# Kernel tuning notes

Hardware: AMD Instinct MI355X
Metric: run time of the kernel (lower is better)

Reference implementation:

```python
import jax, jax.numpy as jnp
import numpy as np

B, S, D = 4, 2048, 1024
LN_EPS = 1e-5
GATE_EPS = 1e-9


def _layernorm(x, g, b):
    m = jnp.mean(x, axis=-1, keepdims=True)
    v = jnp.var(x, axis=-1, keepdims=True)
    return (x - m) * jax.lax.rsqrt(v + LN_EPS) * g + b


def setup_inputs() -> dict:
    key = jax.random.key(0)
    ks = jax.random.split(key, 6)
    return {
        "x": jax.random.normal(ks[0], (B, S, D), jnp.float32),
        "ln1_g": jnp.ones((D,), jnp.float32),
        "ln1_b": jnp.zeros((D,), jnp.float32),
        # stacked per-projection params, order (q, k, v, o)
        "mu_w": 0.02 * jax.random.normal(ks[1], (4, D, D), jnp.float32),
        "mu_b": jnp.zeros((4, D), jnp.float32),
        "proto_w": 0.02 * jax.random.normal(ks[2], (4, D, D), jnp.float32),
        "gate": 0.02 * jax.random.normal(ks[3], (4, D), jnp.float32),
        "pt_w": 0.02 * jax.random.normal(ks[4], (4, D, D), jnp.float32),
        "pln_g": jnp.ones((4, D), jnp.float32),
        "pln_b": jnp.zeros((4, D), jnp.float32),
        "in_proto": 0.02 * jax.random.normal(ks[5], (4, D, D), jnp.float32),
    }


def reference(x, ln1_g, ln1_b, mu_w, mu_b, proto_w, gate, pt_w, pln_g, pln_b, in_proto):
    d = x.shape[-1]
    scale = 1.0 / jnp.sqrt(jnp.asarray(d, x.dtype))

    # proto-state update: proto_weight + LayerNorm(Linear(incoming_proto_state))
    prc = jnp.einsum("ned,nfd->nef", in_proto, pt_w)  # [4,D,D]
    proto_state = proto_w + _layernorm(prc, pln_g[:, None, :], pln_b[:, None, :])

    h = _layernorm(x, ln1_g, ln1_b)  # [B,S,D]

    # SparseProtoLinear for q,k,v (stacked): SiLU GEMM + proto match GEMM
    comp = jax.nn.silu(jnp.einsum("bsd,nfd->nbsf", h, mu_w[:3]) + mu_b[:3, None, None, :])
    mv = jnp.einsum("bsd,nfd->nbsf", h, proto_state[:3]) * scale
    g3 = gate[:3]
    cost = g3 / (jnp.max(jnp.abs(g3), axis=-1, keepdims=True) + GATE_EPS)  # [3,D]
    logits = mv - cost[:, None, None, :]
    masked = comp * (logits > 0)  # hard gate (no grad through mask)
    q, k, v = masked[0], masked[1], masked[2]

    # single-head causal attention, head_dim = d_model
    scores = jnp.einsum("bqd,bkd->bqk", q, k) * scale  # [B,S,S]
    causal = jnp.tril(jnp.ones((scores.shape[-2], scores.shape[-1]), bool))
    scores = jnp.where(causal, scores, jnp.asarray(-jnp.inf, scores.dtype))
    attn = jax.nn.softmax(scores, axis=-1)
    attn_out = jnp.einsum("bqk,bkd->bqd", attn, v)  # [B,S,D]

    # output SparseProtoLinear + gating
    c_o = jax.nn.silu(attn_out @ mu_w[3].T + mu_b[3])
    mv_o = (attn_out @ proto_state[3].T) * scale
    cost_o = gate[3] / (jnp.max(jnp.abs(gate[3])) + GATE_EPS)
    masked_o = c_o * ((mv_o - cost_o) > 0)

    return x + masked_o
```

## Files before the change

### kernel.cpp

```cpp
#include <hip/hip_runtime.h>
#include <math.h>

#define Dd 1024
#define Ss 2048
#define NBATCH 4
#define LDSP 4096

static constexpr size_t SDsz = (size_t)Ss * Dd;
static constexpr size_t MIsz = (size_t)Dd * Dd;
static constexpr size_t SSsz = (size_t)Ss * Ss;
static constexpr float LN_EPS_ = 1e-5f;
static constexpr float GATE_EPS_ = 1e-9f;
static constexpr float SCALE_ = 1.0f / 32.0f;

typedef _Float16 f16;
typedef _Float16 f16x8 __attribute__((ext_vector_type(8)));
typedef _Float16 f16x4 __attribute__((ext_vector_type(4)));
typedef float f32x4 __attribute__((ext_vector_type(4)));

__device__ __forceinline__ float silu_f(float v) { return v / (1.0f + __expf(-v)); }

__device__ __forceinline__ void split2(float x, f16& a, f16& b) {
  a = (f16)x; b = (f16)(x - (float)a);
}

__device__ __forceinline__ int swz(int r, int c) {
  return r * 32 + ((c ^ ((r >> 1) & 3)) << 3);
}

__device__ __forceinline__ float2 block_sum2(float2 v) {
#pragma unroll
  for (int o = 32; o > 0; o >>= 1) { v.x += __shfl_down(v.x, o); v.y += __shfl_down(v.y, o); }
  __shared__ float2 sm2[4];
  if ((threadIdx.x & 63) == 0) sm2[threadIdx.x >> 6] = v;
  __syncthreads();
  float2 r; r.x = sm2[0].x + sm2[1].x + sm2[2].x + sm2[3].x;
  r.y = sm2[0].y + sm2[1].y + sm2[2].y + sm2[3].y;
  __syncthreads();
  return r;
}
__device__ __forceinline__ float block_sum1(float v) {
#pragma unroll
  for (int o = 32; o > 0; o >>= 1) v += __shfl_down(v, o);
  __shared__ float sm1[4];
  if ((threadIdx.x & 63) == 0) sm1[threadIdx.x >> 6] = v;
  __syncthreads();
  float r = sm1[0] + sm1[1] + sm1[2] + sm1[3];
  __syncthreads();
  return r;
}
__device__ __forceinline__ float block_max1(float v) {
#pragma unroll
  for (int o = 32; o > 0; o >>= 1) v = fmaxf(v, __shfl_down(v, o));
  __shared__ float smm[4];
  if ((threadIdx.x & 63) == 0) smm[threadIdx.x >> 6] = v;
  __syncthreads();
  float r = fmaxf(fmaxf(smm[0], smm[1]), fmaxf(smm[2], smm[3]));
  __syncthreads();
  return r;
}

template<int PLANES, int MAXSUM>
__device__ __forceinline__ void mp_core(
    f16* __restrict__ smem,
    const f16* __restrict__ Ap0, const f16* __restrict__ Ap1,
    const f16* __restrict__ Bp0, const f16* __restrict__ Bp1,
    int lda, int ldb, int m0, int n0, int kt_end, f32x4 acc[4][4]) {
  const f16* Ap[2] = {Ap0, Ap1};
  const f16* Bp[2] = {Bp0, Bp1};
  const int tid = threadIdx.x;
  const int l = tid & 63;
  const int wv = tid >> 6;
  const int wr = (wv >> 1) * 64, wc = (wv & 1) * 64;
  const int fl = l & 15, fq = l >> 4;
  const int r0 = tid >> 2, cc = tid & 3, kc = cc * 8;

  f16x8 ra[PLANES][2], rb[PLANES][2];
#pragma unroll
  for (int p = 0; p < PLANES; ++p) {
    ra[p][0] = *(const f16x8*)(Ap[p] + (size_t)(m0 + r0) * lda + kc);
    ra[p][1] = *(const f16x8*)(Ap[p] + (size_t)(m0 + 64 + r0) * lda + kc);
    rb[p][0] = *(const f16x8*)(Bp[p] + (size_t)(n0 + r0) * ldb + kc);
    rb[p][1] = *(const f16x8*)(Bp[p] + (size_t)(n0 + 64 + r0) * ldb + kc);
  }
  for (int kt = 0; kt < kt_end; ++kt) {
    __syncthreads();
#pragma unroll
    for (int p = 0; p < PLANES; ++p) {
      *(f16x8*)(smem + p * LDSP + swz(r0, cc)) = ra[p][0];
      *(f16x8*)(smem + p * LDSP + swz(64 + r0, cc)) = ra[p][1];
      *(f16x8*)(smem + (PLANES + p) * LDSP + swz(r0, cc)) = rb[p][0];
      *(f16x8*)(smem + (PLANES + p) * LDSP + swz(64 + r0, cc)) = rb[p][1];
    }
    __syncthreads();
    if (kt + 1 < kt_end) {
      const int ko = (kt + 1) * 32 + kc;
#pragma unroll
      for (int p = 0; p < PLANES; ++p) {
        ra[p][0] = *(const f16x8*)(Ap[p] + (size_t)(m0 + r0) * lda + ko);
        ra[p][1] = *(const f16x8*)(Ap[p] + (size_t)(m0 + 64 + r0) * lda + ko);
        rb[p][0] = *(const f16x8*)(Bp[p] + (size_t)(n0 + r0) * ldb + ko);
        rb[p][1] = *(const f16x8*)(Bp[p] + (size_t)(n0 + 64 + r0) * ldb + ko);
      }
    }
    f16x8 af[PLANES][4];
#pragma unroll
    for (int p = 0; p < PLANES; ++p)
#pragma unroll
      for (int fr = 0; fr < 4; ++fr)
        af[p][fr] = *(const f16x8*)(smem + p * LDSP + swz(wr + fr * 16 + fl, fq));
#pragma unroll
    for (int fc = 0; fc < 4; ++fc) {
      f16x8 bf[PLANES];
#pragma unroll
      for (int p = 0; p < PLANES; ++p)
        bf[p] = *(const f16x8*)(smem + (PLANES + p) * LDSP + swz(wc + fc * 16 + fl, fq));
#pragma unroll
      for (int i = 0; i < PLANES; ++i)
#pragma unroll
        for (int j = 0; j < PLANES; ++j)
          if (i + j <= MAXSUM) {
#pragma unroll
            for (int fr = 0; fr < 4; ++fr)
              acc[fr][fc] = __builtin_amdgcn_mfma_f32_16x16x32_f16(af[i][fr], bf[j], acc[fr][fc], 0, 0, 0);
          }
    }
  }
}

__device__ __forceinline__ void fused_core(
    f16* __restrict__ smem,
    const f16* __restrict__ A0p, const f16* __restrict__ A1p,
    const f16* __restrict__ W0p, const f16* __restrict__ W1p,
    const f16* __restrict__ P0p, const f16* __restrict__ P1p,
    int lda, int ldb, int m0, int n0, int kt_end,
    f32x4 acc1[4][4], f32x4 acc2[4][4]) {
  const f16* As[2] = {A0p, A1p};
  const f16* Bs[4] = {W0p, W1p, P0p, P1p};
  const int tid = threadIdx.x;
  const int l = tid & 63;
  const int wv = tid >> 6;
  const int wr = (wv >> 1) * 64, wc = (wv & 1) * 64;
  const int fl = l & 15, fq = l >> 4;
  const int r0 = tid >> 2, cc = tid & 3, kc = cc * 8;

  f16x8 ra[2][2], rb[4][2];
#pragma unroll
  for (int p = 0; p < 2; ++p) {
    ra[p][0] = *(const f16x8*)(As[p] + (size_t)(m0 + r0) * lda + kc);
    ra[p][1] = *(const f16x8*)(As[p] + (size_t)(m0 + 64 + r0) * lda + kc);
  }
#pragma unroll
  for (int p = 0; p < 4; ++p) {
    rb[p][0] = *(const f16x8*)(Bs[p] + (size_t)(n0 + r0) * ldb + kc);
    rb[p][1] = *(const f16x8*)(Bs[p] + (size_t)(n0 + 64 + r0) * ldb + kc);
  }
  for (int kt = 0; kt < kt_end; ++kt) {
    __syncthreads();
#pragma unroll
    for (int p = 0; p < 2; ++p) {
      *(f16x8*)(smem + p * LDSP + swz(r0, cc)) = ra[p][0];
      *(f16x8*)(smem + p * LDSP + swz(64 + r0, cc)) = ra[p][1];
    }
#pragma unroll
    for (int p = 0; p < 4; ++p) {
      *(f16x8*)(smem + (2 + p) * LDSP + swz(r0, cc)) = rb[p][0];
      *(f16x8*)(smem + (2 + p) * LDSP + swz(64 + r0, cc)) = rb[p][1];
    }
    __syncthreads();
    if (kt + 1 < kt_end) {
      const int ko = (kt + 1) * 32 + kc;
#pragma unroll
      for (int p = 0; p < 2; ++p) {
        ra[p][0] = *(const f16x8*)(As[p] + (size_t)(m0 + r0) * lda + ko);
        ra[p][1] = *(const f16x8*)(As[p] + (size_t)(m0 + 64 + r0) * lda + ko);
      }
#pragma unroll
      for (int p = 0; p < 4; ++p) {
        rb[p][0] = *(const f16x8*)(Bs[p] + (size_t)(n0 + r0) * ldb + ko);
        rb[p][1] = *(const f16x8*)(Bs[p] + (size_t)(n0 + 64 + r0) * ldb + ko);
      }
    }
    f16x8 af0[4], af1[4];
#pragma unroll
    for (int fr = 0; fr < 4; ++fr) {
      af0[fr] = *(const f16x8*)(smem + 0 * LDSP + swz(wr + fr * 16 + fl, fq));
      af1[fr] = *(const f16x8*)(smem + 1 * LDSP + swz(wr + fr * 16 + fl, fq));
    }
#pragma unroll
    for (int fc = 0; fc < 4; ++fc) {
      f16x8 bw0 = *(const f16x8*)(smem + 2 * LDSP + swz(wc + fc * 16 + fl, fq));
      f16x8 bw1 = *(const f16x8*)(smem + 3 * LDSP + swz(wc + fc * 16 + fl, fq));
      f16x8 bp0 = *(const f16x8*)(smem + 4 * LDSP + swz(wc + fc * 16 + fl, fq));
      f16x8 bp1 = *(const f16x8*)(smem + 5 * LDSP + swz(wc + fc * 16 + fl, fq));
#pragma unroll
      for (int fr = 0; fr < 4; ++fr) {
        acc1[fr][fc] = __builtin_amdgcn_mfma_f32_16x16x32_f16(af0[fr], bw0, acc1[fr][fc], 0, 0, 0);
        acc2[fr][fc] = __builtin_amdgcn_mfma_f32_16x16x32_f16(af0[fr], bp0, acc2[fr][fc], 0, 0, 0);
        acc1[fr][fc] = __builtin_amdgcn_mfma_f32_16x16x32_f16(af0[fr], bw1, acc1[fr][fc], 0, 0, 0);
        acc2[fr][fc] = __builtin_amdgcn_mfma_f32_16x16x32_f16(af0[fr], bp1, acc2[fr][fc], 0, 0, 0);
        acc1[fr][fc] = __builtin_amdgcn_mfma_f32_16x16x32_f16(af1[fr], bw0, acc1[fr][fc], 0, 0, 0);
        acc2[fr][fc] = __builtin_amdgcn_mfma_f32_16x16x32_f16(af1[fr], bp0, acc2[fr][fc], 0, 0, 0);
      }
    }
  }
}

template<class F>
__device__ __forceinline__ void epilogue(const f32x4 acc[4][4], int m0, int n0, F&& f) {
  const int tid = threadIdx.x;
  const int l = tid & 63;
  const int wv = tid >> 6;
  const int wr = (wv >> 1) * 64, wc = (wv & 1) * 64;
  const int fl = l & 15, fq = l >> 4;
#pragma unroll
  for (int fr = 0; fr < 4; ++fr)
#pragma unroll
    for (int fc = 0; fc < 4; ++fc) {
      f32x4 av = acc[fr][fc];
#pragma unroll
      for (int r = 0; r < 4; ++r)
        f(m0 + wr + fr * 16 + fq * 4 + r, n0 + wc + fc * 16 + fl, av[r]);
    }
}
template<class F>
__device__ __forceinline__ void epilogue2(const f32x4 a1[4][4], const f32x4 a2[4][4], int m0, int n0, F&& f) {
  const int tid = threadIdx.x;
  const int l = tid & 63;
  const int wv = tid >> 6;
  const int wr = (wv >> 1) * 64, wc = (wv & 1) * 64;
  const int fl = l & 15, fq = l >> 4;
#pragma unroll
  for (int fr = 0; fr < 4; ++fr)
#pragma unroll
    for (int fc = 0; fc < 4; ++fc) {
      f32x4 v1 = a1[fr][fc], v2 = a2[fr][fc];
#pragma unroll
      for (int r = 0; r < 4; ++r)
        f(m0 + wr + fr * 16 + fq * 4 + r, n0 + wc + fc * 16 + fl, v1[r], v2[r]);
    }
}


__global__ __launch_bounds__(256, 3) void k_prc(const f16* __restrict__ ip0, const f16* __restrict__ ip1,
                                                const f16* __restrict__ pt0, const f16* __restrict__ pt1,
                                                float* __restrict__ prc) {
  __shared__ f16 smem[4 * LDSP];
  const int n = blockIdx.z;
  const int m0 = blockIdx.x * 128, n0 = blockIdx.y * 128;
  const size_t o = (size_t)n * MIsz;
  f32x4 acc[4][4] = {};
  mp_core<2, 2>(smem, ip0 + o, ip1 + o, pt0 + o, pt1 + o, Dd, Dd, m0, n0, Dd / 32, acc);
  float* Cp = prc + o;
  epilogue(acc, m0, n0, [&](int row, int col, float aval) {
    Cp[(size_t)row * Dd + col] = aval;
  });
}

__global__ __launch_bounds__(256, 2) void k_fqkv(const f16* __restrict__ h0, const f16* __restrict__ h1,
                                                 const f16* __restrict__ w0, const f16* __restrict__ w1,
                                                 const f16* __restrict__ s0, const f16* __restrict__ s1,
                                                 const float* __restrict__ mu_b, const float* __restrict__ cost,
                                                 f16* __restrict__ qkvb, int C) {
  __shared__ f16 smem[6 * LDSP];
  const int z = blockIdx.z, n = z / C, cb = z - n * C;
  const int m0 = blockIdx.x * 128, n0 = blockIdx.y * 128;
  const size_t ao = (size_t)cb * SDsz, bo = (size_t)n * MIsz;
  f32x4 acc1[4][4] = {}, acc2[4][4] = {};
  fused_core(smem, h0 + ao, h1 + ao, w0 + bo, w1 + bo, s0 + bo, s1 + bo,
             Dd, Dd, m0, n0, Dd / 32, acc1, acc2);
  const float* bp = mu_b + (size_t)n * Dd;
  const float* cp = cost + (size_t)n * Dd;
  f16* o0 = qkvb + ((size_t)(2 * n) * C + cb) * SDsz;
  f16* o1 = qkvb + ((size_t)(2 * n + 1) * C + cb) * SDsz;
  epilogue2(acc1, acc2, m0, n0, [&](int row, int col, float v1, float v2) {
    bool m = (v2 * SCALE_ - cp[col]) > 0.f;
    float comp = m ? silu_f(v1 + bp[col]) : 0.f;
    f16 lo, hi; split2(comp, lo, hi);
    size_t idx = (size_t)row * Dd + col;
    o0[idx] = lo; o1[idx] = hi;
  });
}

__global__ __launch_bounds__(256, 3) void k_scores(const f16* __restrict__ qkvb, float* __restrict__ scores, int C) {
  const int m0 = blockIdx.x * 128, n0 = blockIdx.y * 128;
  if (n0 >= m0 + 128) return;
  __shared__ f16 smem[4 * LDSP];
  const int cb = blockIdx.z;
  const f16* q0 = qkvb + ((size_t)0 * C + cb) * SDsz;
  const f16* q1 = qkvb + ((size_t)1 * C + cb) * SDsz;
  const f16* kk0 = qkvb + ((size_t)2 * C + cb) * SDsz;
  const f16* kk1 = qkvb + ((size_t)3 * C + cb) * SDsz;
  f32x4 acc[4][4] = {};
  mp_core<2, 1>(smem, q0, q1, kk0, kk1, Dd, Dd, m0, n0, Dd / 32, acc);
  float* Cp = scores + (size_t)cb * SSsz;
  epilogue(acc, m0, n0, [&](int row, int col, float aval) {
    Cp[(size_t)row * Ss + col] = aval * SCALE_;
  });
}

__global__ __launch_bounds__(256, 3) void k_pv(const f16* __restrict__ a0, const f16* __restrict__ a1,
                                               const f16* __restrict__ vT0, const f16* __restrict__ vT1,
                                               f16* __restrict__ ao0, f16* __restrict__ ao1) {
  __shared__ f16 smem[4 * LDSP];
  const int cb = blockIdx.z;
  const int m0 = blockIdx.x * 128, n0 = blockIdx.y * 128;
  const f16* A0 = a0 + (size_t)cb * SSsz;
  const f16* A1 = a1 + (size_t)cb * SSsz;
  const f16* B0 = vT0 + (size_t)cb * SDsz;
  const f16* B1 = vT1 + (size_t)cb * SDsz;
  const int kt_end = (m0 + 128) / 32;
  f32x4 acc[4][4] = {};
  mp_core<2, 1>(smem, A0, A1, B0, B1, Ss, Ss, m0, n0, kt_end, acc);
  f16* p0 = ao0 + (size_t)cb * SDsz;
  f16* p1 = ao1 + (size_t)cb * SDsz;
  epilogue(acc, m0, n0, [&](int row, int col, float aval) {
    f16 x0, x1; split2(aval, x0, x1);
    size_t idx = (size_t)row * Dd + col;
    p0[idx] = x0; p1[idx] = x1;
  });
}

__global__ __launch_bounds__(256, 2) void k_fout(const f16* __restrict__ ao0, const f16* __restrict__ ao1,
                                                 const f16* __restrict__ w30, const f16* __restrict__ w31,
                                                 const f16* __restrict__ s30, const f16* __restrict__ s31,
                                                 const float* __restrict__ b3, const float* __restrict__ cost3,
                                                 const float* __restrict__ x, float* __restrict__ out, int b0) {
  __shared__ f16 smem[6 * LDSP];
  const int cb = blockIdx.z;
  const int m0 = blockIdx.x * 128, n0 = blockIdx.y * 128;
  const size_t ao = (size_t)cb * SDsz;
  f32x4 acc1[4][4] = {}, acc2[4][4] = {};
  fused_core(smem, ao0 + ao, ao1 + ao, w30, w31, s30, s31,
             Dd, Dd, m0, n0, Dd / 32, acc1, acc2);
  const float* xp = x + (size_t)(b0 + cb) * SDsz;
  float* op = out + (size_t)(b0 + cb) * SDsz;
  epilogue2(acc1, acc2, m0, n0, [&](int row, int col, float v1, float v2) {
    size_t idx = (size_t)row * Dd + col;
    bool m = (v2 * SCALE_ - cost3[col]) > 0.f;
    op[idx] = xp[idx] + (m ? silu_f(v1 + b3[col]) : 0.f);
  });
}

__global__ __launch_bounds__(256) void k_cost(const float* __restrict__ gate, float* __restrict__ cost) {
  int n = blockIdx.x;
  const float* g = gate + (size_t)n * Dd;
  float m = 0.f;
  for (int i = threadIdx.x; i < Dd; i += 256) m = fmaxf(m, fabsf(g[i]));
  m = block_max1(m);
  float inv = 1.0f / (m + GATE_EPS_);
  for (int i = threadIdx.x; i < Dd; i += 256) cost[(size_t)n * Dd + i] = g[i] * inv;
}

__global__ __launch_bounds__(256) void k_ln2(const float* __restrict__ x, const float* __restrict__ g,
                                             const float* __restrict__ b, f16* __restrict__ h0,
                                             f16* __restrict__ h1, int b0) {
  size_t row = blockIdx.x;
  const float* xr = x + ((size_t)b0 * Ss + row) * Dd;
  float4 v = ((const float4*)xr)[threadIdx.x];
  float2 s = {v.x + v.y + v.z + v.w, v.x * v.x + v.y * v.y + v.z * v.z + v.w * v.w};
  s = block_sum2(s);
  float mean = s.x * (1.0f / Dd);
  float var = s.y * (1.0f / Dd) - mean * mean;
  float rs = rsqrtf(var + LN_EPS_);
  float4 gg = ((const float4*)g)[threadIdx.x];
  float4 bb = ((const float4*)b)[threadIdx.x];
  float o[4];
  o[0] = (v.x - mean) * rs * gg.x + bb.x;
  o[1] = (v.y - mean) * rs * gg.y + bb.y;
  o[2] = (v.z - mean) * rs * gg.z + bb.z;
  o[3] = (v.w - mean) * rs * gg.w + bb.w;
  f16x4 p0, p1;
#pragma unroll
  for (int j = 0; j < 4; ++j) { f16 a_, b_; split2(o[j], a_, b_); p0[j] = a_; p1[j] = b_; }
  ((f16x4*)(h0 + row * Dd))[threadIdx.x] = p0;
  ((f16x4*)(h1 + row * Dd))[threadIdx.x] = p1;
}

__global__ __launch_bounds__(256) void k_pln2(const float* __restrict__ prc, const float* __restrict__ proto_w,
                                              const float* __restrict__ pg, const float* __restrict__ pb,
                                              f16* __restrict__ s0, f16* __restrict__ s1) {
  size_t row = blockIdx.x;
  int n = (int)(row >> 10);
  float4 v = ((const float4*)(prc + row * Dd))[threadIdx.x];
  float2 s = {v.x + v.y + v.z + v.w, v.x * v.x + v.y * v.y + v.z * v.z + v.w * v.w};
  s = block_sum2(s);
  float mean = s.x * (1.0f / Dd);
  float var = s.y * (1.0f / Dd) - mean * mean;
  float rs = rsqrtf(var + LN_EPS_);
  float4 gg = ((const float4*)(pg + (size_t)n * Dd))[threadIdx.x];
  float4 bb = ((const float4*)(pb + (size_t)n * Dd))[threadIdx.x];
  float4 pw = ((const float4*)(proto_w + row * Dd))[threadIdx.x];
  float o[4];
  o[0] = (v.x - mean) * rs * gg.x + bb.x + pw.x;
  o[1] = (v.y - mean) * rs * gg.y + bb.y + pw.y;
  o[2] = (v.z - mean) * rs * gg.z + bb.z + pw.z;
  o[3] = (v.w - mean) * rs * gg.w + bb.w + pw.w;
  f16x4 p0, p1;
#pragma unroll
  for (int j = 0; j < 4; ++j) { f16 a_, b_; split2(o[j], a_, b_); p0[j] = a_; p1[j] = b_; }
  ((f16x4*)(s0 + row * Dd))[threadIdx.x] = p0;
  ((f16x4*)(s1 + row * Dd))[threadIdx.x] = p1;
}

__global__ __launch_bounds__(256) void k_split2(const float* __restrict__ in, f16* __restrict__ p0,
                                                f16* __restrict__ p1, size_t n4) {
  size_t stride = (size_t)gridDim.x * 256;
  for (size_t i = (size_t)blockIdx.x * 256 + threadIdx.x; i < n4; i += stride) {
    float4 v = ((const float4*)in)[i];
    f16x4 lo, hi;
    f16 a_, b_;
    split2(v.x, a_, b_); lo[0] = a_; hi[0] = b_;
    split2(v.y, a_, b_); lo[1] = a_; hi[1] = b_;
    split2(v.z, a_, b_); lo[2] = a_; hi[2] = b_;
    split2(v.w, a_, b_); lo[3] = a_; hi[3] = b_;
    ((f16x4*)p0)[i] = lo;
    ((f16x4*)p1)[i] = hi;
  }
}

__global__ __launch_bounds__(256) void k_trans(const f16* __restrict__ qkvb, f16* __restrict__ vT0,
                                               f16* __restrict__ vT1, int C) {
  __shared__ f16 t[64][72];
  const int z = blockIdx.z, pl = z & 1, cb = z >> 1;
  const f16* in = qkvb + ((size_t)(4 + pl) * C + cb) * SDsz;
  f16* out = (pl ? vT1 : vT0) + (size_t)cb * SDsz;
  const int s0 = blockIdx.x * 64, d0 = blockIdx.y * 64;
  const int tid = threadIdx.x;
#pragma unroll
  for (int it = 0; it < 2; ++it) {
    int c = tid + it * 256;
    int r = c >> 3, c8 = (c & 7) * 8;
    *(f16x8*)&t[r][c8] = *(const f16x8*)(in + (size_t)(s0 + r) * Dd + d0 + c8);
  }
  __syncthreads();
#pragma unroll
  for (int it = 0; it < 2; ++it) {
    int c = tid + it * 256;
    int r = c >> 3, c8 = (c & 7) * 8;
    f16x8 o;
#pragma unroll
    for (int j = 0; j < 8; ++j) o[j] = t[c8 + j][r];
    *(f16x8*)(out + (size_t)(d0 + r) * Ss + s0 + c8) = o;
  }
}

__global__ __launch_bounds__(256) void k_softmax2(const float* __restrict__ scores, f16* __restrict__ a0,
                                                  f16* __restrict__ a1) {
  const int q = blockIdx.x, cb = blockIdx.z;
  const float* row = scores + (size_t)cb * SSsz + (size_t)q * Ss;
  float4 v0 = ((const float4*)row)[threadIdx.x];
  float4 v1 = ((const float4*)row)[threadIdx.x + 256];
  int b0i = threadIdx.x * 4, b1i = (threadIdx.x + 256) * 4;
  v0.x = (b0i + 0 <= q) ? v0.x : -INFINITY;
  v0.y = (b0i + 1 <= q) ? v0.y : -INFINITY;
  v0.z = (b0i + 2 <= q) ? v0.z : -INFINITY;
  v0.w = (b0i + 3 <= q) ? v0.w : -INFINITY;
  v1.x = (b1i + 0 <= q) ? v1.x : -INFINITY;
  v1.y = (b1i + 1 <= q) ? v1.y : -INFINITY;
  v1.z = (b1i + 2 <= q) ? v1.z : -INFINITY;
  v1.w = (b1i + 3 <= q) ? v1.w : -INFINITY;
  float mx = fmaxf(fmaxf(fmaxf(v0.x, v0.y), fmaxf(v0.z, v0.w)),
                   fmaxf(fmaxf(v1.x, v1.y), fmaxf(v1.z, v1.w)));
  mx = block_max1(mx);
  v0.x = (b0i + 0 <= q) ? __expf(v0.x - mx) : 0.f;
  v0.y = (b0i + 1 <= q) ? __expf(v0.y - mx) : 0.f;
  v0.z = (b0i + 2 <= q) ? __expf(v0.z - mx) : 0.f;
  v0.w = (b0i + 3 <= q) ? __expf(v0.w - mx) : 0.f;
  v1.x = (b1i + 0 <= q) ? __expf(v1.x - mx) : 0.f;
  v1.y = (b1i + 1 <= q) ? __expf(v1.y - mx) : 0.f;
  v1.z = (b1i + 2 <= q) ? __expf(v1.z - mx) : 0.f;
  v1.w = (b1i + 3 <= q) ? __expf(v1.w - mx) : 0.f;
  float s = v0.x + v0.y + v0.z + v0.w + v1.x + v1.y + v1.z + v1.w;
  s = block_sum1(s);
  float inv = 1.0f / s;
  float p0a[4] = {v0.x * inv, v0.y * inv, v0.z * inv, v0.w * inv};
  float p1a[4] = {v1.x * inv, v1.y * inv, v1.z * inv, v1.w * inv};
  f16* r0 = a0 + (size_t)cb * SSsz + (size_t)q * Ss;
  f16* r1 = a1 + (size_t)cb * SSsz + (size_t)q * Ss;
  f16x4 lo0, hi0, lo1, hi1;
#pragma unroll
  for (int j = 0; j < 4; ++j) {
    f16 a_, b_;
    split2(p0a[j], a_, b_); lo0[j] = a_; hi0[j] = b_;
    split2(p1a[j], a_, b_); lo1[j] = a_; hi1[j] = b_;
  }
  ((f16x4*)r0)[threadIdx.x] = lo0;
  ((f16x4*)r0)[threadIdx.x + 256] = lo1;
  ((f16x4*)r1)[threadIdx.x] = hi0;
  ((f16x4*)r1)[threadIdx.x + 256] = hi1;
}

extern "C" void kernel_launch(void* const* d_in, const int* in_sizes, int n_in,
                              void* d_out, int out_size, void* d_ws, size_t ws_size,
                              hipStream_t stream) {
  const float* x        = (const float*)d_in[0];
  const float* ln1_g    = (const float*)d_in[1];
  const float* ln1_b    = (const float*)d_in[2];
  const float* mu_w     = (const float*)d_in[3];
  const float* mu_b     = (const float*)d_in[4];
  const float* proto_w  = (const float*)d_in[5];
  const float* gate     = (const float*)d_in[6];
  const float* pt_w     = (const float*)d_in[7];
  const float* pln_g    = (const float*)d_in[8];
  const float* pln_b    = (const float*)d_in[9];
  const float* in_proto = (const float*)d_in[10];
  float* out = (float*)d_out;

  uint8_t* base = (uint8_t*)d_ws;
  size_t off = 0;
  auto take = [&](size_t b) -> uint8_t* {
    uint8_t* p = base + off;
    off = (off + b + 255) & ~(size_t)255;
    return p;
  };
  const size_t SDb = SDsz * 2;
  f16* w0  = (f16*)take(4 * MIsz * 2);
  f16* w1  = (f16*)take(4 * MIsz * 2);
  f16* ps0 = (f16*)take(4 * MIsz * 2);
  f16* ps1 = (f16*)take(4 * MIsz * 2);
  float* cost = (float*)take(4096 * 4);
  const size_t poolOff = off;

  auto need = [&](int c) -> size_t { return poolOff + (size_t)c * 14 * SDb + (1u << 20); };
  int C = (ws_size >= need(4)) ? 4 : (ws_size >= need(2)) ? 2 : 1;

  uint8_t* pool = base + poolOff;
  f16* h0 = (f16*)pool;
  f16* h1 = h0 + (size_t)C * SDsz;
  uint8_t* Rc = pool + (size_t)2 * C * SDb;
  uint8_t* Rq = Rc + (size_t)6 * C * SDb;
  float* scores = (float*)Rc;
  f16* vT0 = (f16*)(Rc + (size_t)C * SSsz * 4);
  f16* vT1 = vT0 + (size_t)C * SDsz;
  f16* ao0 = (f16*)Rc;
  f16* ao1 = ao0 + (size_t)C * SDsz;
  f16* qkvb = (f16*)Rq;
  f16* a0 = (f16*)Rq;
  f16* a1 = a0 + (size_t)C * SSsz;
  f16* ip0 = (f16*)pool;
  f16* ip1 = ip0 + 4 * MIsz;
  f16* pt0 = ip1 + 4 * MIsz;
  f16* pt1 = pt0 + 4 * MIsz;
  float* prc = (float*)(pool + 4 * (4 * MIsz * 2));

  k_cost<<<dim3(4), dim3(256), 0, stream>>>(gate, cost);
  k_split2<<<dim3(1024), dim3(256), 0, stream>>>(mu_w, w0, w1, MIsz);
  k_split2<<<dim3(1024), dim3(256), 0, stream>>>(in_proto, ip0, ip1, MIsz);
  k_split2<<<dim3(1024), dim3(256), 0, stream>>>(pt_w, pt0, pt1, MIsz);
  k_prc<<<dim3(8, 8, 4), dim3(256), 0, stream>>>(ip0, ip1, pt0, pt1, prc);
  k_pln2<<<dim3(4096), dim3(256), 0, stream>>>(prc, proto_w, pln_g, pln_b, ps0, ps1);

  for (int b0 = 0; b0 < NBATCH; b0 += C) {
    k_ln2<<<dim3(C * Ss), dim3(256), 0, stream>>>(x, ln1_g, ln1_b, h0, h1, b0);
    k_fqkv<<<dim3(16, 8, 3 * C), dim3(256), 0, stream>>>(h0, h1, w0, w1, ps0, ps1,
                                                         mu_b, cost, qkvb, C);
    k_trans<<<dim3(32, 16, 2 * C), dim3(256), 0, stream>>>(qkvb, vT0, vT1, C);
    k_scores<<<dim3(16, 16, C), dim3(256), 0, stream>>>(qkvb, scores, C);
    k_softmax2<<<dim3(Ss, 1, C), dim3(256), 0, stream>>>(scores, a0, a1);
    k_pv<<<dim3(16, 8, C), dim3(256), 0, stream>>>(a0, a1, vT0, vT1, ao0, ao1);
    k_fout<<<dim3(16, 8, C), dim3(256), 0, stream>>>(ao0, ao1,
                                                     w0 + 3 * MIsz, w1 + 3 * MIsz,
                                                     ps0 + 3 * MIsz, ps1 + 3 * MIsz,
                                                     mu_b + 3 * Dd, cost + 3 * Dd, x, out, b0);
  }
}
```

Measured before the change: 789.6 us.

## Fuse softmax normalization into PV GEMM and remap workgroups for XCD locality

The softmax kernel that wrote normalized probabilities as two fp16 split matrices is replaced by a row-statistics kernel that stores only the row max and inverse sum. The PV GEMM now reads the fp32 scores directly, applies exp, normalization and the causal mask in its load path, and splits to hi/lo fp16 before staging into LDS. This removes writing and re-reading two S×S fp16 matrices, at the cost of extra exp work inside the GEMM and a simpler, non-async load pipeline. Separately, the fused QKV and output kernels remap the workgroup index across 8 XCDs so that neighbouring tiles share an L2.

```diff
diff --git a/kernel.cpp b/kernel.cpp
--- a/kernel.cpp
+++ b/kernel.cpp
@@ -263,8 +263,16 @@
                                                  const float* __restrict__ mu_b, const float* __restrict__ cost,
                                                  f16* __restrict__ qkvb, int C) {
   __shared__ f16 smem[6 * LDSP];
-  const int z = blockIdx.z, n = z / C, cb = z - n * C;
-  const int m0 = blockIdx.x * 128, n0 = blockIdx.y * 128;
+  const int nwg = 16 * 8 * gridDim.z;
+  const int f = blockIdx.x + 16 * (blockIdx.y + 8 * blockIdx.z);
+  const int per = nwg >> 3;
+  const int w = (f & 7) * per + (f >> 3);
+  const int mxi = w & 15;
+  const int rest = w >> 4;
+  const int ny = rest & 7;
+  const int z = rest >> 3;
+  const int n = z / C, cb = z - n * C;
+  const int m0 = mxi * 128, n0 = ny * 128;
   const size_t ao = (size_t)cb * SDsz, bo = (size_t)n * MIsz;
   f32x4 acc1[4][4] = {}, acc2[4][4] = {};
   fused_core(smem, h0 + ao, h1 + ao, w0 + bo, w1 + bo, s0 + bo, s1 + bo,
@@ -299,19 +307,123 @@
   });
 }
 
-__global__ __launch_bounds__(256, 3) void k_pv(const f16* __restrict__ a0, const f16* __restrict__ a1,
-                                               const f16* __restrict__ vT0, const f16* __restrict__ vT1,
-                                               f16* __restrict__ ao0, f16* __restrict__ ao1) {
+__global__ __launch_bounds__(256) void k_rowstats(const float* __restrict__ scores, float2* __restrict__ rs) {
+  const int q = blockIdx.x, cb = blockIdx.z;
+  const float* row = scores + (size_t)cb * SSsz + (size_t)q * Ss;
+  float4 v0 = ((const float4*)row)[threadIdx.x];
+  float4 v1 = ((const float4*)row)[threadIdx.x + 256];
+  int b0i = threadIdx.x * 4, b1i = (threadIdx.x + 256) * 4;
+  v0.x = (b0i + 0 <= q) ? v0.x : -INFINITY;
+  v0.y = (b0i + 1 <= q) ? v0.y : -INFINITY;
+  v0.z = (b0i + 2 <= q) ? v0.z : -INFINITY;
+  v0.w = (b0i + 3 <= q) ? v0.w : -INFINITY;
+  v1.x = (b1i + 0 <= q) ? v1.x : -INFINITY;
+  v1.y = (b1i + 1 <= q) ? v1.y : -INFINITY;
+  v1.z = (b1i + 2 <= q) ? v1.z : -INFINITY;
+  v1.w = (b1i + 3 <= q) ? v1.w : -INFINITY;
+  float mx = fmaxf(fmaxf(fmaxf(v0.x, v0.y), fmaxf(v0.z, v0.w)),
+                   fmaxf(fmaxf(v1.x, v1.y), fmaxf(v1.z, v1.w)));
+  mx = block_max1(mx);
+  float s = 0.f;
+  s += (b0i + 0 <= q) ? __expf(v0.x - mx) : 0.f;
+  s += (b0i + 1 <= q) ? __expf(v0.y - mx) : 0.f;
+  s += (b0i + 2 <= q) ? __expf(v0.z - mx) : 0.f;
+  s += (b0i + 3 <= q) ? __expf(v0.w - mx) : 0.f;
+  s += (b1i + 0 <= q) ? __expf(v1.x - mx) : 0.f;
+  s += (b1i + 1 <= q) ? __expf(v1.y - mx) : 0.f;
+  s += (b1i + 2 <= q) ? __expf(v1.z - mx) : 0.f;
+  s += (b1i + 3 <= q) ? __expf(v1.w - mx) : 0.f;
+  s = block_sum1(s);
+  if (threadIdx.x == 0) {
+    float2 o; o.x = mx; o.y = 1.0f / s;
+    rs[(size_t)cb * Ss + q] = o;
+  }
+}
+
+__global__ __launch_bounds__(256, 2) void k_spv(const float* __restrict__ scores, const float2* __restrict__ rs,
+                                                const f16* __restrict__ vT0, const f16* __restrict__ vT1,
+                                                f16* __restrict__ ao0, f16* __restrict__ ao1) {
   __shared__ f16 smem[4 * LDSP];
   const int cb = blockIdx.z;
   const int m0 = blockIdx.x * 128, n0 = blockIdx.y * 128;
-  const f16* A0 = a0 + (size_t)cb * SSsz;
-  const f16* A1 = a1 + (size_t)cb * SSsz;
+  const float* S = scores + (size_t)cb * SSsz;
+  const float2* rss = rs + (size_t)cb * Ss;
   const f16* B0 = vT0 + (size_t)cb * SDsz;
   const f16* B1 = vT1 + (size_t)cb * SDsz;
   const int kt_end = (m0 + 128) / 32;
+
+  const int tid = threadIdx.x;
+  const int l = tid & 63;
+  const int wv = tid >> 6;
+  const int wr = (wv >> 1) * 64, wc = (wv & 1) * 64;
+  const int fl = l & 15, fq = l >> 4;
+  const int r0 = tid >> 2, cc = tid & 3, kc = cc * 8;
+
+  const int row0 = m0 + r0, row1 = m0 + 64 + r0;
+  const float2 st0 = rss[row0];
+  const float2 st1 = rss[row1];
+
+  auto ldP = [&](int row, float2 st, int kbase, f16x8& lo, f16x8& hi) {
+    const float* p = S + (size_t)row * Ss + kbase;
+    float4 sa = *(const float4*)p;
+    float4 sb = *(const float4*)(p + 4);
+    float sv[8] = {sa.x, sa.y, sa.z, sa.w, sb.x, sb.y, sb.z, sb.w};
+#pragma unroll
+    for (int j = 0; j < 8; ++j) {
+      float pv = (kbase + j <= row) ? __expf(sv[j] - st.x) * st.y : 0.f;
+      f16 a_, b_; split2(pv, a_, b_);
+      lo[j] = a_; hi[j] = b_;
+    }
+  };
+
   f32x4 acc[4][4] = {};
-  mp_core<2, 1>(smem, A0, A1, B0, B1, Ss, Ss, m0, n0, kt_end, acc);
+  f16x8 pl[2], ph[2];
+  f16x8 rbv[2][2];
+  ldP(row0, st0, kc, pl[0], ph[0]);
+  ldP(row1, st1, kc, pl[1], ph[1]);
+  rbv[0][0] = *(const f16x8*)(B0 + (size_t)(n0 + r0) * Ss + kc);
+  rbv[0][1] = *(const f16x8*)(B0 + (size_t)(n0 + 64 + r0) * Ss + kc);
+  rbv[1][0] = *(const f16x8*)(B1 + (size_t)(n0 + r0) * Ss + kc);
+  rbv[1][1] = *(const f16x8*)(B1 + (size_t)(n0 + 64 + r0) * Ss + kc);
+
+  for (int kt = 0; kt < kt_end; ++kt) {
+    __syncthreads();
+    *(f16x8*)(smem + 0 * LDSP + swz(r0, cc)) = pl[0];
+    *(f16x8*)(smem + 0 * LDSP + swz(64 + r0, cc)) = pl[1];
+    *(f16x8*)(smem + 1 * LDSP + swz(r0, cc)) = ph[0];
+    *(f16x8*)(smem + 1 * LDSP + swz(64 + r0, cc)) = ph[1];
+    *(f16x8*)(smem + 2 * LDSP + swz(r0, cc)) = rbv[0][0];
+    *(f16x8*)(smem + 2 * LDSP + swz(64 + r0, cc)) = rbv[0][1];
+    *(f16x8*)(smem + 3 * LDSP + swz(r0, cc)) = rbv[1][0];
+    *(f16x8*)(smem + 3 * LDSP + swz(64 + r0, cc)) = rbv[1][1];
+    __syncthreads();
+    if (kt + 1 < kt_end) {
+      const int ko = (kt + 1) * 32 + kc;
+      ldP(row0, st0, ko, pl[0], ph[0]);
+      ldP(row1, st1, ko, pl[1], ph[1]);
+      rbv[0][0] = *(const f16x8*)(B0 + (size_t)(n0 + r0) * Ss + ko);
+      rbv[0][1] = *(const f16x8*)(B0 + (size_t)(n0 + 64 + r0) * Ss + ko);
+      rbv[1][0] = *(const f16x8*)(B1 + (size_t)(n0 + r0) * Ss + ko);
+      rbv[1][1] = *(const f16x8*)(B1 + (size_t)(n0 + 64 + r0) * Ss + ko);
+    }
+    f16x8 af0[4], af1[4];
+#pragma unroll
+    for (int fr = 0; fr < 4; ++fr) {
+      af0[fr] = *(const f16x8*)(smem + 0 * LDSP + swz(wr + fr * 16 + fl, fq));
+      af1[fr] = *(const f16x8*)(smem + 1 * LDSP + swz(wr + fr * 16 + fl, fq));
+    }
+#pragma unroll
+    for (int fc = 0; fc < 4; ++fc) {
+      f16x8 bf0 = *(const f16x8*)(smem + 2 * LDSP + swz(wc + fc * 16 + fl, fq));
+      f16x8 bf1 = *(const f16x8*)(smem + 3 * LDSP + swz(wc + fc * 16 + fl, fq));
+#pragma unroll
+      for (int fr = 0; fr < 4; ++fr) {
+        acc[fr][fc] = __builtin_amdgcn_mfma_f32_16x16x32_f16(af0[fr], bf0, acc[fr][fc], 0, 0, 0);
+        acc[fr][fc] = __builtin_amdgcn_mfma_f32_16x16x32_f16(af0[fr], bf1, acc[fr][fc], 0, 0, 0);
+        acc[fr][fc] = __builtin_amdgcn_mfma_f32_16x16x32_f16(af1[fr], bf0, acc[fr][fc], 0, 0, 0);
+      }
+    }
+  }
   f16* p0 = ao0 + (size_t)cb * SDsz;
   f16* p1 = ao1 + (size_t)cb * SDsz;
   epilogue(acc, m0, n0, [&](int row, int col, float aval) {
@@ -327,8 +439,15 @@
                                                  const float* __restrict__ b3, const float* __restrict__ cost3,
                                                  const float* __restrict__ x, float* __restrict__ out, int b0) {
   __shared__ f16 smem[6 * LDSP];
-  const int cb = blockIdx.z;
-  const int m0 = blockIdx.x * 128, n0 = blockIdx.y * 128;
+  const int nwg = 16 * 8 * gridDim.z;
+  const int f = blockIdx.x + 16 * (blockIdx.y + 8 * blockIdx.z);
+  const int per = nwg >> 3;
+  const int w = (f & 7) * per + (f >> 3);
+  const int mxi = w & 15;
+  const int rest = w >> 4;
+  const int ny = rest & 7;
+  const int cb = rest >> 3;
+  const int m0 = mxi * 128, n0 = ny * 128;
   const size_t ao = (size_t)cb * SDsz;
   f32x4 acc1[4][4] = {}, acc2[4][4] = {};
   fused_core(smem, ao0 + ao, ao1 + ao, w30, w31, s30, s31,
@@ -445,52 +564,6 @@
   }
 }
 
-__global__ __launch_bounds__(256) void k_softmax2(const float* __restrict__ scores, f16* __restrict__ a0,
-                                                  f16* __restrict__ a1) {
-  const int q = blockIdx.x, cb = blockIdx.z;
-  const float* row = scores + (size_t)cb * SSsz + (size_t)q * Ss;
-  float4 v0 = ((const float4*)row)[threadIdx.x];
-  float4 v1 = ((const float4*)row)[threadIdx.x + 256];
-  int b0i = threadIdx.x * 4, b1i = (threadIdx.x + 256) * 4;
-  v0.x = (b0i + 0 <= q) ? v0.x : -INFINITY;
-  v0.y = (b0i + 1 <= q) ? v0.y : -INFINITY;
-  v0.z = (b0i + 2 <= q) ? v0.z : -INFINITY;
-  v0.w = (b0i + 3 <= q) ? v0.w : -INFINITY;
-  v1.x = (b1i + 0 <= q) ? v1.x : -INFINITY;
-  v1.y = (b1i + 1 <= q) ? v1.y : -INFINITY;
-  v1.z = (b1i + 2 <= q) ? v1.z : -INFINITY;
-  v1.w = (b1i + 3 <= q) ? v1.w : -INFINITY;
-  float mx = fmaxf(fmaxf(fmaxf(v0.x, v0.y), fmaxf(v0.z, v0.w)),
-                   fmaxf(fmaxf(v1.x, v1.y), fmaxf(v1.z, v1.w)));
-  mx = block_max1(mx);
-  v0.x = (b0i + 0 <= q) ? __expf(v0.x - mx) : 0.f;
-  v0.y = (b0i + 1 <= q) ? __expf(v0.y - mx) : 0.f;
-  v0.z = (b0i + 2 <= q) ? __expf(v0.z - mx) : 0.f;
-  v0.w = (b0i + 3 <= q) ? __expf(v0.w - mx) : 0.f;
-  v1.x = (b1i + 0 <= q) ? __expf(v1.x - mx) : 0.f;
-  v1.y = (b1i + 1 <= q) ? __expf(v1.y - mx) : 0.f;
-  v1.z = (b1i + 2 <= q) ? __expf(v1.z - mx) : 0.f;
-  v1.w = (b1i + 3 <= q) ? __expf(v1.w - mx) : 0.f;
-  float s = v0.x + v0.y + v0.z + v0.w + v1.x + v1.y + v1.z + v1.w;
-  s = block_sum1(s);
-  float inv = 1.0f / s;
-  float p0a[4] = {v0.x * inv, v0.y * inv, v0.z * inv, v0.w * inv};
-  float p1a[4] = {v1.x * inv, v1.y * inv, v1.z * inv, v1.w * inv};
-  f16* r0 = a0 + (size_t)cb * SSsz + (size_t)q * Ss;
-  f16* r1 = a1 + (size_t)cb * SSsz + (size_t)q * Ss;
-  f16x4 lo0, hi0, lo1, hi1;
-#pragma unroll
-  for (int j = 0; j < 4; ++j) {
-    f16 a_, b_;
-    split2(p0a[j], a_, b_); lo0[j] = a_; hi0[j] = b_;
-    split2(p1a[j], a_, b_); lo1[j] = a_; hi1[j] = b_;
-  }
-  ((f16x4*)r0)[threadIdx.x] = lo0;
-  ((f16x4*)r0)[threadIdx.x + 256] = lo1;
-  ((f16x4*)r1)[threadIdx.x] = hi0;
-  ((f16x4*)r1)[threadIdx.x + 256] = hi1;
-}
-
 extern "C" void kernel_launch(void* const* d_in, const int* in_sizes, int n_in,
                               void* d_out, int out_size, void* d_ws, size_t ws_size,
                               hipStream_t stream) {
@@ -520,6 +593,7 @@
   f16* ps0 = (f16*)take(4 * MIsz * 2);
   f16* ps1 = (f16*)take(4 * MIsz * 2);
   float* cost = (float*)take(4096 * 4);
+  float2* rs = (float2*)take(4 * (size_t)Ss * sizeof(float2));
   const size_t poolOff = off;
 
   auto need = [&](int c) -> size_t { return poolOff + (size_t)c * 14 * SDb + (1u << 20); };
@@ -533,11 +607,9 @@
   float* scores = (float*)Rc;
   f16* vT0 = (f16*)(Rc + (size_t)C * SSsz * 4);
   f16* vT1 = vT0 + (size_t)C * SDsz;
-  f16* ao0 = (f16*)Rc;
+  f16* qkvb = (f16*)Rq;
+  f16* ao0 = (f16*)Rq;
   f16* ao1 = ao0 + (size_t)C * SDsz;
-  f16* qkvb = (f16*)Rq;
-  f16* a0 = (f16*)Rq;
-  f16* a1 = a0 + (size_t)C * SSsz;
   f16* ip0 = (f16*)pool;
   f16* ip1 = ip0 + 4 * MIsz;
   f16* pt0 = ip1 + 4 * MIsz;
@@ -557,8 +629,8 @@
                                                          mu_b, cost, qkvb, C);
     k_trans<<<dim3(32, 16, 2 * C), dim3(256), 0, stream>>>(qkvb, vT0, vT1, C);
     k_scores<<<dim3(16, 16, C), dim3(256), 0, stream>>>(qkvb, scores, C);
-    k_softmax2<<<dim3(Ss, 1, C), dim3(256), 0, stream>>>(scores, a0, a1);
-    k_pv<<<dim3(16, 8, C), dim3(256), 0, stream>>>(a0, a1, vT0, vT1, ao0, ao1);
+    k_rowstats<<<dim3(Ss, 1, C), dim3(256), 0, stream>>>(scores, rs);
+    k_spv<<<dim3(16, 8, C), dim3(256), 0, stream>>>(scores, rs, vT0, vT1, ao0, ao1);
     k_fout<<<dim3(16, 8, C), dim3(256), 0, stream>>>(ao0, ao1,
                                                      w0 + 3 * MIsz, w1 + 3 * MIsz,
                                                      ps0 + 3 * MIsz, ps1 + 3 * MIsz,
```

New measurement: 845.1 us. 1.07x slower.
